# Optimization experiments

Measured on AMD Instinct MI355X. Metric: run time of the kernel, lower is better.

Reference implementation:

```python
import jax, jax.numpy as jnp
import numpy as np

N, S, T, E, H = 4, 2048, 2048, 512, 8
HD = E // H  # head_dim = 64


def setup_inputs() -> dict:
    key0 = jax.random.key(0)
    ks = jax.random.split(key0, 12)
    sc = 1.0 / np.sqrt(E)
    inp = {
        "query": jax.random.normal(ks[0], (N, S, E), jnp.float32),
        "key": jax.random.normal(ks[1], (N, T, E), jnp.float32),
        "value": jax.random.normal(ks[2], (N, T, E), jnp.float32),
        "attn_mask": jnp.tril(jnp.ones((S, T), jnp.int32)),  # causal: 0 => masked
        # nn.Linear weights (out, in) and biases, torch convention y = x @ W.T + b
        "Wq": jax.random.normal(ks[3], (E, E), jnp.float32) * sc,
        "bq": jax.random.normal(ks[4], (E,), jnp.float32) * sc,
        "Wk": jax.random.normal(ks[5], (E, E), jnp.float32) * sc,
        "bk": jax.random.normal(ks[6], (E,), jnp.float32) * sc,
        "Wv": jax.random.normal(ks[7], (E, E), jnp.float32) * sc,
        "bv": jax.random.normal(ks[8], (E,), jnp.float32) * sc,
        "Wp": jax.random.normal(ks[9], (E, E), jnp.float32) * sc,
        "bp": jax.random.normal(ks[10], (E,), jnp.float32) * sc,
    }
    return inp


def reference(query, key, value, attn_mask, Wq, bq, Wk, bk, Wv, bv, Wp, bp):
    # QKV projections, split heads: (N, H, L, HD)
    q = (query @ Wq.T + bq).reshape(N, S, H, HD).transpose(0, 2, 1, 3)
    k = (key @ Wk.T + bk).reshape(N, T, H, HD).transpose(0, 2, 1, 3)
    v = (value @ Wv.T + bv).reshape(N, T, H, HD).transpose(0, 2, 1, 3)
    # scaled scores (N, H, S, T) -- intentionally materialized like the original
    e = jnp.einsum("nhsd,nhtd->nhst", q, k) / jnp.sqrt(jnp.float32(HD))
    e = jnp.where(attn_mask == 0, -jnp.inf, e)
    a = jax.nn.softmax(e, axis=-1)
    # dropout is identity in eval mode (reference runs deterministic/eval)
    y = jnp.einsum("nhst,nhtd->nhsd", a, v)
    y = y.transpose(0, 2, 1, 3).reshape(N, S, E)
    return y @ Wp.T + bp
```

## Files before the change

kernel.cpp:

```cpp
#include <hip/hip_runtime.h>


#define DEV __device__ __forceinline__

typedef unsigned short u16;
typedef unsigned int u32;
typedef __bf16 bf16x8 __attribute__((ext_vector_type(8)));
typedef float f32x4 __attribute__((ext_vector_type(4)));
typedef u32 u32x4 __attribute__((ext_vector_type(4)));

#define MFMA_BF16(A, B, C) __builtin_amdgcn_mfma_f32_16x16x32_bf16(A, B, C, 0, 0, 0)

DEV u16 f2bf(float f) {
  u32 u = __builtin_bit_cast(u32, f);
  u += 0x7fffu + ((u >> 16) & 1u);
  return (u16)(u >> 16);
}

DEV void cp16(void* l, const void* g) {
  __builtin_amdgcn_global_load_lds(
      (const __attribute__((address_space(1))) u32*)g,
      (__attribute__((address_space(3))) u32*)l, 16, 0, 0);
}

__global__ __launch_bounds__(256) void cast3(const float* __restrict__ q,
                                             const float* __restrict__ k,
                                             const float* __restrict__ v,
                                             u16* qo, u16* ko, u16* vo) {
  const float* s = (blockIdx.y == 0) ? q : (blockIdx.y == 1) ? k : v;
  u16* d = (blockIdx.y == 0) ? qo : (blockIdx.y == 1) ? ko : vo;
  int i = blockIdx.x * 256 + threadIdx.x;
  float4 f = ((const float4*)s)[i];
  ushort4 o;
  o.x = f2bf(f.x); o.y = f2bf(f.y); o.z = f2bf(f.z); o.w = f2bf(f.w);
  ((ushort4*)d)[i] = o;
}

__global__ __launch_bounds__(256) void cast4(const float* __restrict__ a,
                                             const float* __restrict__ b,
                                             const float* __restrict__ c,
                                             const float* __restrict__ d2,
                                             u16* ao, u16* bo, u16* co, u16* do_) {
  int y = blockIdx.y;
  const float* s = (y == 0) ? a : (y == 1) ? b : (y == 2) ? c : d2;
  u16* d = (y == 0) ? ao : (y == 1) ? bo : (y == 2) ? co : do_;
  int i = blockIdx.x * 256 + threadIdx.x;
  float4 f = ((const float4*)s)[i];
  ushort4 o;
  o.x = f2bf(f.x); o.y = f2bf(f.y); o.z = f2bf(f.z); o.w = f2bf(f.w);
  ((ushort4*)d)[i] = o;
}

DEV void gemm_loop(const u16* __restrict__ A, const u16* __restrict__ W,
                   u16* As, u16* Bs, int m0, int n0, int tid, f32x4 acc[4][4]) {
  const int lane = tid & 63, wid = tid >> 6;
  const int wm = wid & 1, wn = wid >> 1;
  const int l15 = lane & 15, l4 = lane >> 4;
  for (int kt = 0; kt < 512; kt += 32) {
    __syncthreads();
#pragma unroll
    for (int i = 0; i < 2; ++i) {
      int c = tid + 256 * i;
      int row = c >> 2, kc = (c & 3) * 8;
      cp16(&As[c * 8], A + (m0 + row) * 512 + kt + kc);
      cp16(&Bs[c * 8], W + (n0 + row) * 512 + kt + kc);
    }
    __syncthreads();
    bf16x8 af[4], bfr[4];
#pragma unroll
    for (int f = 0; f < 4; ++f) {
      af[f]  = *(const bf16x8*)&As[(wm * 64 + f * 16 + l15) * 32 + l4 * 8];
      bfr[f] = *(const bf16x8*)&Bs[(wn * 64 + f * 16 + l15) * 32 + l4 * 8];
    }
#pragma unroll
    for (int fm = 0; fm < 4; ++fm)
#pragma unroll
      for (int fn = 0; fn < 4; ++fn)
        acc[fm][fn] = MFMA_BF16(af[fm], bfr[fn], acc[fm][fn]);
  }
}

__global__ __launch_bounds__(256) void gemm_qkv(
    const u16* __restrict__ qx, const u16* __restrict__ kx, const u16* __restrict__ vx,
    const u16* __restrict__ wq, const u16* __restrict__ wk, const u16* __restrict__ wv,
    const float* __restrict__ bq, const float* __restrict__ bk, const float* __restrict__ bv,
    u16* qp, u16* kp, u16* vp) {
  __shared__ u16 As[128 * 32];
  __shared__ u16 Bs[128 * 32];
  const int wsel = blockIdx.x >> 2;
  const u16* A = (wsel == 0) ? qx : (wsel == 1) ? kx : vx;
  const u16* W = (wsel == 0) ? wq : (wsel == 1) ? wk : wv;
  const float* bias = (wsel == 0) ? bq : (wsel == 1) ? bk : bv;
  u16* C = (wsel == 0) ? qp : (wsel == 1) ? kp : vp;
  const int n0 = (blockIdx.x & 3) * 128, m0 = blockIdx.y * 128;
  const int tid = threadIdx.x, lane = tid & 63, wid = tid >> 6;
  const int wm = wid & 1, wn = wid >> 1;
  const int l15 = lane & 15, l4 = lane >> 4;
  const float osc = (wsel == 0) ? 0.18033688f : 1.0f;

  f32x4 acc[4][4] = {};
  gemm_loop(A, W, As, Bs, m0, n0, tid, acc);

#pragma unroll
  for (int fn = 0; fn < 4; ++fn) {
    int col = n0 + wn * 64 + fn * 16 + l15;
    float bvv = bias[col];
#pragma unroll
    for (int fm = 0; fm < 4; ++fm) {
      int rowb = m0 + wm * 64 + fm * 16 + l4 * 4;
#pragma unroll
      for (int r = 0; r < 4; ++r)
        C[(rowb + r) * 512 + col] = f2bf((acc[fm][fn][r] + bvv) * osc);
    }
  }
}

__global__ __launch_bounds__(256) void gemm_out(const u16* __restrict__ A,
                                                const u16* __restrict__ W,
                                                const float* __restrict__ bias,
                                                float* __restrict__ C) {
  __shared__ u16 As[64 * 32];
  __shared__ u16 Bs[128 * 32];
  const int n0 = blockIdx.x * 128, m0 = blockIdx.y * 64;
  const int tid = threadIdx.x, lane = tid & 63, wid = tid >> 6;
  const int wm = wid & 1, wn = wid >> 1;
  const int l15 = lane & 15, l4 = lane >> 4;

  f32x4 acc[2][4] = {};
  for (int kt = 0; kt < 512; kt += 32) {
    __syncthreads();
    {
      int row = tid >> 2, kc = (tid & 3) * 8;
      cp16(&As[tid * 8], A + (m0 + row) * 512 + kt + kc);
    }
#pragma unroll
    for (int i = 0; i < 2; ++i) {
      int c = tid + 256 * i;
      int row = c >> 2, kc = (c & 3) * 8;
      cp16(&Bs[c * 8], W + (n0 + row) * 512 + kt + kc);
    }
    __syncthreads();
    bf16x8 af[2], bfr[4];
#pragma unroll
    for (int f = 0; f < 2; ++f)
      af[f] = *(const bf16x8*)&As[(wm * 32 + f * 16 + l15) * 32 + l4 * 8];
#pragma unroll
    for (int f = 0; f < 4; ++f)
      bfr[f] = *(const bf16x8*)&Bs[(wn * 64 + f * 16 + l15) * 32 + l4 * 8];
#pragma unroll
    for (int fm = 0; fm < 2; ++fm)
#pragma unroll
      for (int fn = 0; fn < 4; ++fn)
        acc[fm][fn] = MFMA_BF16(af[fm], bfr[fn], acc[fm][fn]);
  }

#pragma unroll
  for (int fn = 0; fn < 4; ++fn) {
    int col = n0 + wn * 64 + fn * 16 + l15;
    float bvv = bias[col];
#pragma unroll
    for (int fm = 0; fm < 2; ++fm) {
      int rowb = m0 + wm * 32 + fm * 16 + l4 * 4;
#pragma unroll
      for (int r = 0; r < 4; ++r)
        C[(rowb + r) * 512 + col] = acc[fm][fn][r] + bvv;
    }
  }
}

__global__ __launch_bounds__(256) void transpose_v(const u16* __restrict__ vp,
                                                   u16* __restrict__ vt) {
  __shared__ u16 L[64 * 72];
  const int bid = blockIdx.x;
  const int nh = bid & 31, tt = bid >> 5;
  const int n = nh >> 3, h = nh & 7;
  const u16* src = vp + (n * 2048 + tt * 64) * 512 + h * 64;
  const int tid = threadIdx.x;
#pragma unroll
  for (int i = 0; i < 2; ++i) {
    int c = tid + 256 * i;
    int row = c >> 3, dg = c & 7;
    uint4 x = *(const uint4*)(src + row * 512 + dg * 8);
    *(uint4*)&L[row * 72 + dg * 8] = x;
  }
  __syncthreads();
  u16* dst = vt + nh * 64 * 2048 + tt * 64;
#pragma unroll
  for (int i = 0; i < 2; ++i) {
    int c = tid + 256 * i;
    int d = c >> 3, tg = c & 7;
    u16 e[8];
#pragma unroll
    for (int j = 0; j < 8; ++j) e[j] = L[(tg * 8 + j) * 72 + d];
    uint4 o;
    o.x = (u32)e[0] | ((u32)e[1] << 16);
    o.y = (u32)e[2] | ((u32)e[3] << 16);
    o.z = (u32)e[4] | ((u32)e[5] << 16);
    o.w = (u32)e[6] | ((u32)e[7] << 16);
    *(uint4*)(dst + d * 2048 + tg * 8) = o;
  }
}

__global__ __launch_bounds__(256) void attn_kernel(const u16* __restrict__ Qg,
                                                   const u16* __restrict__ Kg,
                                                   const u16* __restrict__ Vt,
                                                   u16* __restrict__ Yg) {
  __shared__ u16 Qs[64 * 64];
  __shared__ u16 Ks[128 * 64];
  __shared__ u16 Vts[64 * 128];

  const int bid = blockIdx.x;
  const int nh = bid & 31;
  const int qt = 31 - (bid >> 5);
  const int n = nh >> 3, h = nh & 7;
  const int tid = threadIdx.x, lane = tid & 63, w = tid >> 6;
  const int l15 = lane & 15, l4 = lane >> 4;
  const int s0 = qt * 64;

  const u16* Qb = Qg + (n * 2048 + s0) * 512 + h * 64;
  const u16* Kb = Kg + n * 2048 * 512 + h * 64;
  const u16* Vb = Vt + nh * 64 * 2048;

#pragma unroll
  for (int i = 0; i < 2; ++i) {
    int c = tid + 256 * i;
    int row = c >> 3, dg = (c & 7) ^ (row & 7);
    cp16(&Qs[c * 8], Qb + row * 512 + dg * 8);
  }
  __syncthreads();
  const int qr = w * 16 + l15;
  bf16x8 qf0 = *(const bf16x8*)&Qs[qr * 64 + ((l4 ^ (qr & 7)) * 8)];
  bf16x8 qf1 = *(const bf16x8*)&Qs[qr * 64 + (((4 + l4) ^ (qr & 7)) * 8)];

  f32x4 accO[4] = {};
  float mrow = -1e30f, lrow = 0.f;
  const int sgl = s0 + w * 16 + l15;

  const int ntiles = (qt >> 1) + 1;
  for (int it = 0; it < ntiles; ++it) {
    const int t0 = it * 128;
    __syncthreads();
#pragma unroll
    for (int i = 0; i < 4; ++i) {
      int c = tid + 256 * i;
      int t = c >> 3, dg = (c & 7) ^ (t & 7);
      cp16(&Ks[c * 8], Kb + (t0 + t) * 512 + dg * 8);
    }
#pragma unroll
    for (int i = 0; i < 4; ++i) {
      int c = tid + 256 * i;
      int d = c >> 4, tgs = c & 15;
      cp16(&Vts[c * 8], Vb + d * 2048 + t0 + ((tgs ^ (d & 15)) * 8));
    }
    __syncthreads();

    f32x4 st[8];
    __builtin_amdgcn_s_setprio(1);
#pragma unroll
    for (int fn = 0; fn < 8; ++fn) {
      int tr = fn * 16 + l15;
      bf16x8 k0 = *(const bf16x8*)&Ks[tr * 64 + ((l4 ^ (tr & 7)) * 8)];
      bf16x8 k1 = *(const bf16x8*)&Ks[tr * 64 + (((4 + l4) ^ (tr & 7)) * 8)];
      f32x4 a = {};
      a = MFMA_BF16(k0, qf0, a);
      st[fn] = MFMA_BF16(k1, qf1, a);
    }
    __builtin_amdgcn_s_setprio(0);

    const bool diag = (t0 + 128 > s0);
    float rmax = -1e30f;
#pragma unroll
    for (int fn = 0; fn < 8; ++fn)
#pragma unroll
      for (int r = 0; r < 4; ++r) {
        float v = st[fn][r];
        if (diag) {
          int tg = t0 + fn * 16 + l4 * 4 + r;
          if (tg > sgl) v = -1e30f;
        }
        st[fn][r] = v;
        rmax = fmaxf(rmax, v);
      }
    rmax = fmaxf(rmax, __shfl_xor(rmax, 16));
    rmax = fmaxf(rmax, __shfl_xor(rmax, 32));
    if (__any(rmax > mrow + 10.f)) {
      float mnew = fmaxf(mrow, rmax);
      float alpha = __builtin_amdgcn_exp2f(mrow - mnew);
      mrow = mnew;
      lrow *= alpha;
      float aO[4];
#pragma unroll
      for (int r = 0; r < 4; ++r) aO[r] = __shfl(alpha, (lane & 48) | (l4 * 4 + r));
#pragma unroll
      for (int fd = 0; fd < 4; ++fd)
#pragma unroll
        for (int r = 0; r < 4; ++r) accO[fd][r] *= aO[r];
    }
    float rsum = 0.f;
#pragma unroll
    for (int fn = 0; fn < 8; ++fn)
#pragma unroll
      for (int r = 0; r < 4; ++r) {
        float p = __builtin_amdgcn_exp2f(st[fn][r] - mrow);
        st[fn][r] = p;
        rsum += p;
      }
    rsum += __shfl_xor(rsum, 16);
    rsum += __shfl_xor(rsum, 32);
    lrow += rsum;

    bf16x8 pa[4];
#pragma unroll
    for (int ks = 0; ks < 4; ++ks) {
      bf16x8 t;
      t[0] = (__bf16)st[2 * ks][0];     t[1] = (__bf16)st[2 * ks][1];
      t[2] = (__bf16)st[2 * ks][2];     t[3] = (__bf16)st[2 * ks][3];
      t[4] = (__bf16)st[2 * ks + 1][0]; t[5] = (__bf16)st[2 * ks + 1][1];
      t[6] = (__bf16)st[2 * ks + 1][2]; t[7] = (__bf16)st[2 * ks + 1][3];
      pa[ks] = t;
    }

    __builtin_amdgcn_s_setprio(1);
#pragma unroll
    for (int ks = 0; ks < 4; ++ks) {
#pragma unroll
      for (int fd = 0; fd < 4; ++fd) {
        int d = fd * 16 + l15;
        const u16* vrow = &Vts[d * 128];
        uint2 v0 = *(const uint2*)&vrow[(((ks * 4 + (l4 >> 1)) ^ l15) * 8) + (l4 & 1) * 4];
        uint2 v1 = *(const uint2*)&vrow[(((ks * 4 + 2 + (l4 >> 1)) ^ l15) * 8) + (l4 & 1) * 4];
        u32x4 bw; bw.x = v0.x; bw.y = v0.y; bw.z = v1.x; bw.w = v1.y;
        accO[fd] = MFMA_BF16(pa[ks], __builtin_bit_cast(bf16x8, bw), accO[fd]);
      }
    }
    __builtin_amdgcn_s_setprio(0);
  }

  float lO[4];
#pragma unroll
  for (int r = 0; r < 4; ++r) lO[r] = __shfl(lrow, (lane & 48) | (l4 * 4 + r));
#pragma unroll
  for (int fd = 0; fd < 4; ++fd)
#pragma unroll
    for (int r = 0; r < 4; ++r) {
      int row = s0 + w * 16 + l4 * 4 + r;
      int col = h * 64 + fd * 16 + l15;
      Yg[(n * 2048 + row) * 512 + col] = f2bf(accO[fd][r] / lO[r]);
    }
}

extern "C" void kernel_launch(void* const* d_in, const int* in_sizes, int n_in,
                              void* d_out, int out_size, void* d_ws, size_t ws_size,
                              hipStream_t stream) {
  (void)in_sizes; (void)n_in; (void)out_size; (void)ws_size;
  const float* query = (const float*)d_in[0];
  const float* key_  = (const float*)d_in[1];
  const float* value = (const float*)d_in[2];
  const float* Wq = (const float*)d_in[4];
  const float* bq = (const float*)d_in[5];
  const float* Wk = (const float*)d_in[6];
  const float* bk = (const float*)d_in[7];
  const float* Wv = (const float*)d_in[8];
  const float* bv = (const float*)d_in[9];
  const float* Wp = (const float*)d_in[10];
  const float* bp = (const float*)d_in[11];

  char* ws = (char*)d_ws;
  u16* qx  = (u16*)(ws);
  u16* kx  = (u16*)(ws + 8388608);
  u16* vx  = (u16*)(ws + 16777216);
  u16* wqx = (u16*)(ws + 25165824);
  u16* wkx = (u16*)(ws + 25690112);
  u16* wvx = (u16*)(ws + 26214400);
  u16* wpx = (u16*)(ws + 26738688);
  u16* qp  = (u16*)(ws + 27262976);
  u16* kp  = (u16*)(ws + 35651584);
  u16* vp  = (u16*)(ws + 44040192);
  u16* y   = qx;
  u16* vt  = kx;

  cast3<<<dim3(4096, 3), 256, 0, stream>>>(query, key_, value, qx, kx, vx);
  cast4<<<dim3(256, 4), 256, 0, stream>>>(Wq, Wk, Wv, Wp, wqx, wkx, wvx, wpx);

  gemm_qkv<<<dim3(12, 64), 256, 0, stream>>>(qx, kx, vx, wqx, wkx, wvx,
                                             bq, bk, bv, qp, kp, vp);
  transpose_v<<<1024, 256, 0, stream>>>(vp, vt);
  attn_kernel<<<1024, 256, 0, stream>>>(qp, kp, vt, y);
  gemm_out<<<dim3(4, 128), 256, 0, stream>>>(y, wpx, bp, (float*)d_out);
}
```

Baseline: 204.1 us.

## Double-buffer GEMM tiles, pipeline K/V loads in attention, merge cast kernels

The QKV and output GEMMs now use double-buffered LDS with explicit waitcnt and barrier, so the next k-tile is prefetched while MFMAs run on the current one. The attention kernel issues the K and V loads for the next tile right after each stage consumes its buffer, overlapping global loads with compute. The V transpose is reordered so the PV step reads one 16-byte vector instead of two 8-byte loads. The two cast kernels are merged into one launch. This doubles GEMM shared memory and depends on hand-written vmcnt counts being exactly right.

Result: faster. 195.2 us (-4.4%).

```diff
diff --git a/kernel.cpp b/kernel.cpp
--- a/kernel.cpp
+++ b/kernel.cpp
@@ -7,7 +7,6 @@
 typedef unsigned int u32;
 typedef __bf16 bf16x8 __attribute__((ext_vector_type(8)));
 typedef float f32x4 __attribute__((ext_vector_type(4)));
-typedef u32 u32x4 __attribute__((ext_vector_type(4)));
 
 #define MFMA_BF16(A, B, C) __builtin_amdgcn_mfma_f32_16x16x32_bf16(A, B, C, 0, 0, 0)
 
@@ -23,60 +22,76 @@
       (__attribute__((address_space(3))) u32*)l, 16, 0, 0);
 }
 
-__global__ __launch_bounds__(256) void cast3(const float* __restrict__ q,
-                                             const float* __restrict__ k,
-                                             const float* __restrict__ v,
-                                             u16* qo, u16* ko, u16* vo) {
-  const float* s = (blockIdx.y == 0) ? q : (blockIdx.y == 1) ? k : v;
-  u16* d = (blockIdx.y == 0) ? qo : (blockIdx.y == 1) ? ko : vo;
-  int i = blockIdx.x * 256 + threadIdx.x;
+#define WAIT_VM(N) asm volatile("s_waitcnt vmcnt(" #N ")" ::: "memory")
+#define WAIT_VMLG  asm volatile("s_waitcnt vmcnt(0) lgkmcnt(0)" ::: "memory")
+#define WAIT_LG    asm volatile("s_waitcnt lgkmcnt(0)" ::: "memory")
+#define BARRIER    asm volatile("s_barrier" ::: "memory")
+
+__global__ __launch_bounds__(256) void cast_all(
+    const float* __restrict__ q, const float* __restrict__ k, const float* __restrict__ v,
+    const float* __restrict__ wq, const float* __restrict__ wk,
+    const float* __restrict__ wv, const float* __restrict__ wp,
+    u16* qo, u16* ko, u16* vo, u16* wqo, u16* wko, u16* wvo, u16* wpo) {
+  int b = blockIdx.x;
+  const float* s;
+  u16* d;
+  int i;
+  if (b < 12288) {
+    int t = b >> 12;
+    s = (t == 0) ? q : (t == 1) ? k : v;
+    d = (t == 0) ? qo : (t == 1) ? ko : vo;
+    i = (b & 4095) * 256 + threadIdx.x;
+  } else {
+    int t = (b - 12288) >> 8;
+    s = (t == 0) ? wq : (t == 1) ? wk : (t == 2) ? wv : wp;
+    d = (t == 0) ? wqo : (t == 1) ? wko : (t == 2) ? wvo : wpo;
+    i = ((b - 12288) & 255) * 256 + threadIdx.x;
+  }
   float4 f = ((const float4*)s)[i];
   ushort4 o;
   o.x = f2bf(f.x); o.y = f2bf(f.y); o.z = f2bf(f.z); o.w = f2bf(f.w);
   ((ushort4*)d)[i] = o;
 }
 
-__global__ __launch_bounds__(256) void cast4(const float* __restrict__ a,
-                                             const float* __restrict__ b,
-                                             const float* __restrict__ c,
-                                             const float* __restrict__ d2,
-                                             u16* ao, u16* bo, u16* co, u16* do_) {
-  int y = blockIdx.y;
-  const float* s = (y == 0) ? a : (y == 1) ? b : (y == 2) ? c : d2;
-  u16* d = (y == 0) ? ao : (y == 1) ? bo : (y == 2) ? co : do_;
-  int i = blockIdx.x * 256 + threadIdx.x;
-  float4 f = ((const float4*)s)[i];
-  ushort4 o;
-  o.x = f2bf(f.x); o.y = f2bf(f.y); o.z = f2bf(f.z); o.w = f2bf(f.w);
-  ((ushort4*)d)[i] = o;
+DEV void gemm_stage(const u16* __restrict__ A, const u16* __restrict__ W,
+                    u16* As, u16* Bs, int m0, int n0, int kt, int tid) {
+#pragma unroll
+  for (int i = 0; i < 2; ++i) {
+    int c = tid + 256 * i;
+    int row = c >> 2, kc = (c & 3) * 8;
+    cp16(&As[c * 8], A + (m0 + row) * 512 + kt + kc);
+    cp16(&Bs[c * 8], W + (n0 + row) * 512 + kt + kc);
+  }
 }
 
 DEV void gemm_loop(const u16* __restrict__ A, const u16* __restrict__ W,
-                   u16* As, u16* Bs, int m0, int n0, int tid, f32x4 acc[4][4]) {
+                   u16* As, u16* Bs,
+                   int m0, int n0, int tid, f32x4 acc[4][4]) {
   const int lane = tid & 63, wid = tid >> 6;
   const int wm = wid & 1, wn = wid >> 1;
   const int l15 = lane & 15, l4 = lane >> 4;
-  for (int kt = 0; kt < 512; kt += 32) {
-    __syncthreads();
-#pragma unroll
-    for (int i = 0; i < 2; ++i) {
-      int c = tid + 256 * i;
-      int row = c >> 2, kc = (c & 3) * 8;
-      cp16(&As[c * 8], A + (m0 + row) * 512 + kt + kc);
-      cp16(&Bs[c * 8], W + (n0 + row) * 512 + kt + kc);
-    }
-    __syncthreads();
+  gemm_stage(A, W, As, Bs, m0, n0, 0, tid);
+  for (int it = 0; it < 16; ++it) {
+    WAIT_VMLG;
+    BARRIER;
+    const u16* Ac = As + (it & 1) * 4096;
+    const u16* Bc = Bs + (it & 1) * 4096;
+    if (it < 15)
+      gemm_stage(A, W, As + ((it + 1) & 1) * 4096, Bs + ((it + 1) & 1) * 4096,
+                 m0, n0, (it + 1) * 32, tid);
     bf16x8 af[4], bfr[4];
 #pragma unroll
     for (int f = 0; f < 4; ++f) {
-      af[f]  = *(const bf16x8*)&As[(wm * 64 + f * 16 + l15) * 32 + l4 * 8];
-      bfr[f] = *(const bf16x8*)&Bs[(wn * 64 + f * 16 + l15) * 32 + l4 * 8];
-    }
+      af[f]  = *(const bf16x8*)&Ac[(wm * 64 + f * 16 + l15) * 32 + l4 * 8];
+      bfr[f] = *(const bf16x8*)&Bc[(wn * 64 + f * 16 + l15) * 32 + l4 * 8];
+    }
+    __builtin_amdgcn_s_setprio(1);
 #pragma unroll
     for (int fm = 0; fm < 4; ++fm)
 #pragma unroll
       for (int fn = 0; fn < 4; ++fn)
         acc[fm][fn] = MFMA_BF16(af[fm], bfr[fn], acc[fm][fn]);
+    __builtin_amdgcn_s_setprio(0);
   }
 }
 
@@ -85,8 +100,8 @@
     const u16* __restrict__ wq, const u16* __restrict__ wk, const u16* __restrict__ wv,
     const float* __restrict__ bq, const float* __restrict__ bk, const float* __restrict__ bv,
     u16* qp, u16* kp, u16* vp) {
-  __shared__ u16 As[128 * 32];
-  __shared__ u16 Bs[128 * 32];
+  __shared__ u16 As[2 * 128 * 32];
+  __shared__ u16 Bs[2 * 128 * 32];
   const int wsel = blockIdx.x >> 2;
   const u16* A = (wsel == 0) ? qx : (wsel == 1) ? kx : vx;
   const u16* W = (wsel == 0) ? wq : (wsel == 1) ? wk : wv;
@@ -119,39 +134,49 @@
                                                 const u16* __restrict__ W,
                                                 const float* __restrict__ bias,
                                                 float* __restrict__ C) {
-  __shared__ u16 As[64 * 32];
-  __shared__ u16 Bs[128 * 32];
+  __shared__ u16 As[2 * 64 * 32];
+  __shared__ u16 Bs[2 * 128 * 32];
   const int n0 = blockIdx.x * 128, m0 = blockIdx.y * 64;
   const int tid = threadIdx.x, lane = tid & 63, wid = tid >> 6;
   const int wm = wid & 1, wn = wid >> 1;
   const int l15 = lane & 15, l4 = lane >> 4;
 
-  f32x4 acc[2][4] = {};
-  for (int kt = 0; kt < 512; kt += 32) {
-    __syncthreads();
+  auto stage = [&](u16* Asb, u16* Bsb, int kt) {
     {
       int row = tid >> 2, kc = (tid & 3) * 8;
-      cp16(&As[tid * 8], A + (m0 + row) * 512 + kt + kc);
+      cp16(&Asb[tid * 8], A + (m0 + row) * 512 + kt + kc);
     }
 #pragma unroll
     for (int i = 0; i < 2; ++i) {
       int c = tid + 256 * i;
       int row = c >> 2, kc = (c & 3) * 8;
-      cp16(&Bs[c * 8], W + (n0 + row) * 512 + kt + kc);
-    }
-    __syncthreads();
+      cp16(&Bsb[c * 8], W + (n0 + row) * 512 + kt + kc);
+    }
+  };
+
+  f32x4 acc[2][4] = {};
+  stage(As, Bs, 0);
+  for (int it = 0; it < 16; ++it) {
+    WAIT_VMLG;
+    BARRIER;
+    const u16* Ac = As + (it & 1) * 2048;
+    const u16* Bc = Bs + (it & 1) * 4096;
+    if (it < 15)
+      stage(As + ((it + 1) & 1) * 2048, Bs + ((it + 1) & 1) * 4096, (it + 1) * 32);
     bf16x8 af[2], bfr[4];
 #pragma unroll
     for (int f = 0; f < 2; ++f)
-      af[f] = *(const bf16x8*)&As[(wm * 32 + f * 16 + l15) * 32 + l4 * 8];
+      af[f] = *(const bf16x8*)&Ac[(wm * 32 + f * 16 + l15) * 32 + l4 * 8];
 #pragma unroll
     for (int f = 0; f < 4; ++f)
-      bfr[f] = *(const bf16x8*)&Bs[(wn * 64 + f * 16 + l15) * 32 + l4 * 8];
+      bfr[f] = *(const bf16x8*)&Bc[(wn * 64 + f * 16 + l15) * 32 + l4 * 8];
+    __builtin_amdgcn_s_setprio(1);
 #pragma unroll
     for (int fm = 0; fm < 2; ++fm)
 #pragma unroll
       for (int fn = 0; fn < 4; ++fn)
         acc[fm][fn] = MFMA_BF16(af[fm], bfr[fn], acc[fm][fn]);
+    __builtin_amdgcn_s_setprio(0);
   }
 
 #pragma unroll
@@ -191,7 +216,10 @@
     int d = c >> 3, tg = c & 7;
     u16 e[8];
 #pragma unroll
-    for (int j = 0; j < 8; ++j) e[j] = L[(tg * 8 + j) * 72 + d];
+    for (int j = 0; j < 8; ++j) {
+      int tsrc = (tg & 4) * 8 + (tg & 3) * 4 + (j & 3) + (j >> 2) * 16;
+      e[j] = L[tsrc * 72 + d];
+    }
     uint4 o;
     o.x = (u32)e[0] | ((u32)e[1] << 16);
     o.y = (u32)e[2] | ((u32)e[3] << 16);
@@ -227,7 +255,20 @@
     int row = c >> 3, dg = (c & 7) ^ (row & 7);
     cp16(&Qs[c * 8], Qb + row * 512 + dg * 8);
   }
-  __syncthreads();
+#pragma unroll
+  for (int i = 0; i < 4; ++i) {
+    int c = tid + 256 * i;
+    int t = c >> 3, dg = (c & 7) ^ (t & 7);
+    cp16(&Ks[c * 8], Kb + t * 512 + dg * 8);
+  }
+#pragma unroll
+  for (int i = 0; i < 4; ++i) {
+    int c = tid + 256 * i;
+    int d = c >> 4, x = c & 15;
+    cp16(&Vts[c * 8], Vb + d * 2048 + ((x ^ (d & 15)) * 8));
+  }
+  WAIT_VM(8);
+  BARRIER;
   const int qr = w * 16 + l15;
   bf16x8 qf0 = *(const bf16x8*)&Qs[qr * 64 + ((l4 ^ (qr & 7)) * 8)];
   bf16x8 qf1 = *(const bf16x8*)&Qs[qr * 64 + (((4 + l4) ^ (qr & 7)) * 8)];
@@ -239,20 +280,10 @@
   const int ntiles = (qt >> 1) + 1;
   for (int it = 0; it < ntiles; ++it) {
     const int t0 = it * 128;
-    __syncthreads();
-#pragma unroll
-    for (int i = 0; i < 4; ++i) {
-      int c = tid + 256 * i;
-      int t = c >> 3, dg = (c & 7) ^ (t & 7);
-      cp16(&Ks[c * 8], Kb + (t0 + t) * 512 + dg * 8);
-    }
-#pragma unroll
-    for (int i = 0; i < 4; ++i) {
-      int c = tid + 256 * i;
-      int d = c >> 4, tgs = c & 15;
-      cp16(&Vts[c * 8], Vb + d * 2048 + t0 + ((tgs ^ (d & 15)) * 8));
-    }
-    __syncthreads();
+    const bool more = (it + 1 < ntiles);
+
+    WAIT_VM(4);
+    BARRIER;
 
     f32x4 st[8];
     __builtin_amdgcn_s_setprio(1);
@@ -266,6 +297,17 @@
       st[fn] = MFMA_BF16(k1, qf1, a);
     }
     __builtin_amdgcn_s_setprio(0);
+
+    WAIT_LG;
+    BARRIER;
+    if (more) {
+#pragma unroll
+      for (int i = 0; i < 4; ++i) {
+        int c = tid + 256 * i;
+        int t = c >> 3, dg = (c & 7) ^ (t & 7);
+        cp16(&Ks[c * 8], Kb + (t0 + 128 + t) * 512 + dg * 8);
+      }
+    }
 
     const bool diag = (t0 + 128 > s0);
     float rmax = -1e30f;
@@ -320,20 +362,32 @@
       pa[ks] = t;
     }
 
+    if (more) { WAIT_VM(4); }
+    else      { WAIT_VM(0); }
+    BARRIER;
+
     __builtin_amdgcn_s_setprio(1);
 #pragma unroll
     for (int ks = 0; ks < 4; ++ks) {
 #pragma unroll
       for (int fd = 0; fd < 4; ++fd) {
         int d = fd * 16 + l15;
-        const u16* vrow = &Vts[d * 128];
-        uint2 v0 = *(const uint2*)&vrow[(((ks * 4 + (l4 >> 1)) ^ l15) * 8) + (l4 & 1) * 4];
-        uint2 v1 = *(const uint2*)&vrow[(((ks * 4 + 2 + (l4 >> 1)) ^ l15) * 8) + (l4 & 1) * 4];
-        u32x4 bw; bw.x = v0.x; bw.y = v0.y; bw.z = v1.x; bw.w = v1.y;
-        accO[fd] = MFMA_BF16(pa[ks], __builtin_bit_cast(bf16x8, bw), accO[fd]);
+        bf16x8 bv = *(const bf16x8*)&Vts[d * 128 + (((ks * 4 + l4) ^ l15) * 8)];
+        accO[fd] = MFMA_BF16(pa[ks], bv, accO[fd]);
       }
     }
     __builtin_amdgcn_s_setprio(0);
+
+    WAIT_LG;
+    BARRIER;
+    if (more) {
+#pragma unroll
+      for (int i = 0; i < 4; ++i) {
+        int c = tid + 256 * i;
+        int d = c >> 4, x = c & 15;
+        cp16(&Vts[c * 8], Vb + d * 2048 + (t0 + 128) + ((x ^ (d & 15)) * 8));
+      }
+    }
   }
 
   float lO[4];
@@ -379,9 +433,8 @@
   u16* y   = qx;
   u16* vt  = kx;
 
-  cast3<<<dim3(4096, 3), 256, 0, stream>>>(query, key_, value, qx, kx, vx);
-  cast4<<<dim3(256, 4), 256, 0, stream>>>(Wq, Wk, Wv, Wp, wqx, wkx, wvx, wpx);
-
+  cast_all<<<13312, 256, 0, stream>>>(query, key_, value, Wq, Wk, Wv, Wp,
+                                      qx, kx, vx, wqx, wkx, wvx, wpx);
   gemm_qkv<<<dim3(12, 64), 256, 0, stream>>>(qx, kx, vx, wqx, wkx, wvx,
                                              bq, bk, bv, qp, kp, vp);
   transpose_v<<<1024, 256, 0, stream>>>(vp, vt);
```
